# Kernel optimization log

Hardware: AMD Instinct MI355X
Metric: run time of the kernel (lower is better)

The kernel has to match this reference:

```python
import jax, jax.numpy as jnp
import numpy as np

LR = 0.01  # constraint relaxation learning rate (module default)
EPS = 1e-6


def setup_inputs() -> dict:
    key = jax.random.key(0)
    k1, k2, k3, k4 = jax.random.split(key, 4)
    N, E, K = 8192, 262144, 65536
    positions = jax.random.normal(k1, (N, 3), dtype=jnp.float32)
    edge_index = jax.random.randint(k2, (2, E), 0, N, dtype=jnp.int32)
    dist_idx = jax.random.randint(k3, (K, 2), 0, N, dtype=jnp.int32)
    dist_target = jax.random.uniform(k4, (K,), dtype=jnp.float32) * 2.0
    min_dist = jnp.ones((1,), dtype=jnp.float32) * 0.5
    return {"positions": positions, "edge_index": edge_index,
            "dist_idx": dist_idx, "dist_target": dist_target,
            "min_dist": min_dist}


def reference(positions, edge_index, dist_idx, dist_target, min_dist):
    x = positions  # (N, 3)
    N = x.shape[0]

    # --- distance constraints: ||x_i - x_j|| -> d_ij (Jacobi-style update) ---
    i, j = dist_idx[:, 0], dist_idx[:, 1]
    vec = x[i] - x[j]                                  # (K, 3)
    dist = jnp.sqrt(jnp.sum(vec * vec, axis=-1) + 1e-12)
    valid = (dist > EPS) & (i != j)
    coef = jnp.where(valid, LR * 0.5 * (dist - dist_target) / dist, 0.0)
    corr = coef[:, None] * vec                         # (K, 3)
    x = x.at[i].add(-corr).at[j].add(corr)

    # --- collision constraints: push apart all pairs with dist < min_dist ---
    md = min_dist[0]
    sq = jnp.sum(x * x, axis=-1)                       # (N,)
    d2 = jnp.maximum(sq[:, None] + sq[None, :] - 2.0 * (x @ x.T), 1e-12)
    dmat = jnp.sqrt(d2)                                # (N, N) pairwise distances
    mask = (dmat < md) & (dmat > EPS)                  # excludes diagonal (dist ~ 0)
    w = jnp.where(mask, (md - dmat) / dmat, 0.0) * (0.5 * LR)  # (N, N)
    # correction_i = sum_j w_ij * (x_i - x_j)
    x = x + x * jnp.sum(w, axis=-1, keepdims=True) - w @ x

    # --- gaussian curvature via normalized graph Laplacian ---
    e = jnp.clip(edge_index, 0, N - 1)
    adj = jnp.zeros((N, N), dtype=x.dtype).at[e[0], e[1]].set(1.0)
    adj = adj + adj.T
    deg = adj.sum(axis=1)
    dinv = jnp.where(deg == 0, 0.0, jnp.power(deg + EPS, -0.5))
    # L_norm @ x = x - D^{-1/2} A D^{-1/2} x (diagonal scaling, same math)
    lap = x - dinv[:, None] * (adj @ (dinv[:, None] * x))
    curvature = jnp.sqrt(jnp.sum(lap * lap, axis=-1) + 1e-12)  # (N,)

    return x, curvature
```

## Files before the change

### kernel.cpp

```cpp
#include <hip/hip_runtime.h>
#include <math.h>

#define N_NODES 8192
#define WPR 256
#define LR_C 0.01f
#define EPS_C 1e-6f

__global__ void scatter_constraints(const float* __restrict__ x0,
                                    const int* __restrict__ dist_idx,
                                    const float* __restrict__ dist_target,
                                    float* __restrict__ x1, int K) {
    int k = blockIdx.x * blockDim.x + threadIdx.x;
    if (k >= K) return;
    int i = dist_idx[2 * k], j = dist_idx[2 * k + 1];
    float ax = x0[3 * i], ay = x0[3 * i + 1], az = x0[3 * i + 2];
    float bx = x0[3 * j], by = x0[3 * j + 1], bz = x0[3 * j + 2];
    float vx = ax - bx, vy = ay - by, vz = az - bz;
    float dist = sqrtf(vx * vx + vy * vy + vz * vz + 1e-12f);
    bool valid = (dist > EPS_C) && (i != j);
    float coef = valid ? (LR_C * 0.5f) * (dist - dist_target[k]) / dist : 0.0f;
    if (coef != 0.0f) {
        float cx = coef * vx, cy = coef * vy, cz = coef * vz;
        atomicAdd(&x1[3 * i],     -cx);
        atomicAdd(&x1[3 * i + 1], -cy);
        atomicAdd(&x1[3 * i + 2], -cz);
        atomicAdd(&x1[3 * j],      cx);
        atomicAdd(&x1[3 * j + 1],  cy);
        atomicAdd(&x1[3 * j + 2],  cz);
    }
}

__global__ __launch_bounds__(256) void repulsion_partial(
        const float* __restrict__ x1, const float* __restrict__ min_dist,
        float4* __restrict__ partials) {
    __shared__ float4 pj[256];
    int t = threadIdx.x;
    int jbase = blockIdx.y * 256;
    int i = blockIdx.x * 256 + t;
    {
        int j = jbase + t;
        float a = x1[3 * j], b = x1[3 * j + 1], c = x1[3 * j + 2];
        pj[t] = make_float4(a, b, c, a * a + b * b + c * c);
    }
    __syncthreads();
    float xi = x1[3 * i], yi = x1[3 * i + 1], zi = x1[3 * i + 2];
    float sqi = xi * xi + yi * yi + zi * zi;
    float md = min_dist[0];
    float md2 = md * md;
    const float c0 = 0.5f * LR_C;
    float c1 = c0 * md;
    int di = i - jbase;
    float S = 0.f, axc = 0.f, ayc = 0.f, azc = 0.f;
    #pragma unroll 4
    for (int jj = 0; jj < 256; ++jj) {
        float4 p = pj[jj];
        float dot = fmaf(xi, p.x, fmaf(yi, p.y, zi * p.z));
        float d2 = fmaxf(fmaf(-2.0f, dot, sqi + p.w), 1e-12f);
        float r = __builtin_amdgcn_rsqf(d2);
        bool m = (d2 < md2) && (d2 > 1e-12f) && (jj != di);
        float w = m ? fmaf(c1, r, -c0) : 0.0f;
        S += w;
        axc = fmaf(w, p.x, axc);
        ayc = fmaf(w, p.y, ayc);
        azc = fmaf(w, p.z, azc);
    }
    partials[blockIdx.y * N_NODES + i] = make_float4(axc, ayc, azc, S);
}

__global__ void repulsion_finalize(const float* __restrict__ x1,
                                   const float4* __restrict__ partials,
                                   float* __restrict__ x2,
                                   float* __restrict__ out_x, int nchunks) {
    int i = blockIdx.x * blockDim.x + threadIdx.x;
    if (i >= N_NODES) return;
    float S = 0.f, axc = 0.f, ayc = 0.f, azc = 0.f;
    for (int c = 0; c < nchunks; ++c) {
        float4 p = partials[c * N_NODES + i];
        axc += p.x; ayc += p.y; azc += p.z; S += p.w;
    }
    float xi = x1[3 * i], yi = x1[3 * i + 1], zi = x1[3 * i + 2];
    float ox = xi + xi * S - axc;
    float oy = yi + yi * S - ayc;
    float oz = zi + zi * S - azc;
    x2[3 * i] = ox; x2[3 * i + 1] = oy; x2[3 * i + 2] = oz;
    out_x[3 * i] = ox; out_x[3 * i + 1] = oy; out_x[3 * i + 2] = oz;
}

__global__ void build_adj(const int* __restrict__ edge_index,
                          unsigned int* __restrict__ A,
                          unsigned int* __restrict__ B, int E) {
    int k = blockIdx.x * blockDim.x + threadIdx.x;
    if (k >= E) return;
    int a = edge_index[k];
    int b = edge_index[E + k];
    a = min(max(a, 0), N_NODES - 1);
    b = min(max(b, 0), N_NODES - 1);
    atomicOr(&A[a * WPR + (b >> 5)], 1u << (b & 31));
    atomicOr(&B[b * WPR + (a >> 5)], 1u << (a & 31));
}

__global__ __launch_bounds__(256) void degree_kernel(
        const unsigned int* __restrict__ A, const unsigned int* __restrict__ B,
        const float* __restrict__ x2, float* __restrict__ dinv,
        float4* __restrict__ z4) {
    int row = (blockIdx.x * blockDim.x + threadIdx.x) >> 6;
    int lane = threadIdx.x & 63;
    if (row >= N_NODES) return;
    const unsigned int* ra = A + (size_t)row * WPR;
    const unsigned int* rb = B + (size_t)row * WPR;
    int cnt = 0;
    #pragma unroll
    for (int q = 0; q < 4; ++q) {
        cnt += __popc(ra[q * 64 + lane]);
        cnt += __popc(rb[q * 64 + lane]);
    }
    for (int off = 32; off; off >>= 1) cnt += __shfl_down(cnt, off);
    if (lane == 0) {
        float dv = (cnt == 0) ? 0.0f : 1.0f / sqrtf((float)cnt + EPS_C);
        dinv[row] = dv;
        z4[row] = make_float4(dv * x2[3 * row], dv * x2[3 * row + 1],
                              dv * x2[3 * row + 2], dv);
    }
}

__global__ __launch_bounds__(256) void lap_kernel(
        const unsigned int* __restrict__ A, const unsigned int* __restrict__ B,
        const float* __restrict__ x2, const float* __restrict__ dinv,
        const float4* __restrict__ z4, float* __restrict__ out_curv) {
    int row = (blockIdx.x * blockDim.x + threadIdx.x) >> 6;
    int lane = threadIdx.x & 63;
    if (row >= N_NODES) return;
    float axc = 0.f, ayc = 0.f, azc = 0.f;
    #pragma unroll
    for (int q = 0; q < 4; ++q) {
        int wi = q * 64 + lane;
        unsigned int w = A[(size_t)row * WPR + wi];
        while (w) {
            int b = __ffs(w) - 1; w &= w - 1;
            float4 z = z4[wi * 32 + b];
            axc += z.x; ayc += z.y; azc += z.z;
        }
        w = B[(size_t)row * WPR + wi];
        while (w) {
            int b = __ffs(w) - 1; w &= w - 1;
            float4 z = z4[wi * 32 + b];
            axc += z.x; ayc += z.y; azc += z.z;
        }
    }
    for (int off = 32; off; off >>= 1) {
        axc += __shfl_down(axc, off);
        ayc += __shfl_down(ayc, off);
        azc += __shfl_down(azc, off);
    }
    if (lane == 0) {
        float dv = dinv[row];
        float lx = x2[3 * row]     - dv * axc;
        float ly = x2[3 * row + 1] - dv * ayc;
        float lz = x2[3 * row + 2] - dv * azc;
        out_curv[row] = sqrtf(lx * lx + ly * ly + lz * lz + 1e-12f);
    }
}

extern "C" void kernel_launch(void* const* d_in, const int* in_sizes, int n_in,
                              void* d_out, int out_size, void* d_ws, size_t ws_size,
                              hipStream_t stream) {
    const float* positions   = (const float*)d_in[0];
    const int*   edge_index  = (const int*)d_in[1];
    const int*   dist_idx    = (const int*)d_in[2];
    const float* dist_target = (const float*)d_in[3];
    const float* min_dist    = (const float*)d_in[4];
    float* out = (float*)d_out;

    const int E = in_sizes[1] / 2;
    const int K = in_sizes[2] / 2;
    const int NJ = 32;

    char* ws = (char*)d_ws;
    const size_t X1_OFF   = 0;
    const size_t X2_OFF   = X1_OFF + (size_t)N_NODES * 3 * 4;
    const size_t Z4_OFF   = X2_OFF + (size_t)N_NODES * 3 * 4;
    const size_t DINV_OFF = Z4_OFF + (size_t)N_NODES * 16;
    const size_t PART_OFF = DINV_OFF + (size_t)N_NODES * 4;
    const size_t ADJ_OFF  = PART_OFF + (size_t)NJ * N_NODES * 16;
    const size_t ADJ_BYTES = (size_t)N_NODES * WPR * 4;

    float* x1         = (float*)(ws + X1_OFF);
    float* x2         = (float*)(ws + X2_OFF);
    float4* z4        = (float4*)(ws + Z4_OFF);
    float* dinv       = (float*)(ws + DINV_OFF);
    float4* partials  = (float4*)(ws + PART_OFF);
    unsigned int* A   = (unsigned int*)(ws + ADJ_OFF);
    unsigned int* B   = (unsigned int*)(ws + ADJ_OFF + ADJ_BYTES);

    hipMemcpyAsync(x1, positions, (size_t)N_NODES * 3 * 4,
                   hipMemcpyDeviceToDevice, stream);
    hipMemsetAsync(A, 0, 2 * ADJ_BYTES, stream);

    scatter_constraints<<<(K + 255) / 256, 256, 0, stream>>>(
        positions, dist_idx, dist_target, x1, K);

    dim3 grid_rep(N_NODES / 256, NJ);
    repulsion_partial<<<grid_rep, 256, 0, stream>>>(x1, min_dist, partials);

    repulsion_finalize<<<N_NODES / 256, 256, 0, stream>>>(
        x1, partials, x2, out, NJ);

    build_adj<<<(E + 255) / 256, 256, 0, stream>>>(edge_index, A, B, E);

    int rows_per_block = 256 / 64;
    int nblk = N_NODES / rows_per_block;
    degree_kernel<<<nblk, 256, 0, stream>>>(A, B, x2, dinv, z4);
    lap_kernel<<<nblk, 256, 0, stream>>>(A, B, x2, dinv, z4, out + 3 * N_NODES);
}
```

Measured before the change: 103.3 us.

## Fuse init memcpy/memset into one kernel and merge finalize with degree

Replaces the device memcpy and memset with a single init kernel that zeroes the adjacency bitmaps and copies positions. It also fuses the repulsion partial-sum reduction into the degree kernel, using a wave-wide shuffle reduction over the 32 chunk partials, and moves build_adj earlier. The aim is fewer launches and less per-launch overhead. The init kernel relies on hardcoded sizes (4096*256 uint4 covers both bitmaps, and 6144 float4 covers the positions).

```diff
diff --git a/kernel.cpp b/kernel.cpp
--- a/kernel.cpp
+++ b/kernel.cpp
@@ -5,6 +5,14 @@
 #define WPR 256
 #define LR_C 0.01f
 #define EPS_C 1e-6f
+
+__global__ __launch_bounds__(256) void init_clear(const float4* __restrict__ pos4,
+                                                  float4* __restrict__ x1_4,
+                                                  uint4* __restrict__ adj) {
+    int gid = blockIdx.x * blockDim.x + threadIdx.x;
+    adj[gid] = make_uint4(0u, 0u, 0u, 0u);
+    if (gid < 6144) x1_4[gid] = pos4[gid];
+}
 
 __global__ void scatter_constraints(const float* __restrict__ x0,
                                     const int* __restrict__ dist_idx,
@@ -30,6 +38,19 @@
     }
 }
 
+__global__ void build_adj(const int* __restrict__ edge_index,
+                          unsigned int* __restrict__ A,
+                          unsigned int* __restrict__ B, int E) {
+    int k = blockIdx.x * blockDim.x + threadIdx.x;
+    if (k >= E) return;
+    int a = edge_index[k];
+    int b = edge_index[E + k];
+    a = min(max(a, 0), N_NODES - 1);
+    b = min(max(b, 0), N_NODES - 1);
+    atomicOr(&A[a * WPR + (b >> 5)], 1u << (b & 31));
+    atomicOr(&B[b * WPR + (a >> 5)], 1u << (a & 31));
+}
+
 __global__ __launch_bounds__(256) void repulsion_partial(
         const float* __restrict__ x1, const float* __restrict__ min_dist,
         float4* __restrict__ partials) {
@@ -67,59 +88,43 @@
     partials[blockIdx.y * N_NODES + i] = make_float4(axc, ayc, azc, S);
 }
 
-__global__ void repulsion_finalize(const float* __restrict__ x1,
-                                   const float4* __restrict__ partials,
-                                   float* __restrict__ x2,
-                                   float* __restrict__ out_x, int nchunks) {
-    int i = blockIdx.x * blockDim.x + threadIdx.x;
-    if (i >= N_NODES) return;
-    float S = 0.f, axc = 0.f, ayc = 0.f, azc = 0.f;
-    for (int c = 0; c < nchunks; ++c) {
-        float4 p = partials[c * N_NODES + i];
-        axc += p.x; ayc += p.y; azc += p.z; S += p.w;
-    }
-    float xi = x1[3 * i], yi = x1[3 * i + 1], zi = x1[3 * i + 2];
-    float ox = xi + xi * S - axc;
-    float oy = yi + yi * S - ayc;
-    float oz = zi + zi * S - azc;
-    x2[3 * i] = ox; x2[3 * i + 1] = oy; x2[3 * i + 2] = oz;
-    out_x[3 * i] = ox; out_x[3 * i + 1] = oy; out_x[3 * i + 2] = oz;
-}
-
-__global__ void build_adj(const int* __restrict__ edge_index,
-                          unsigned int* __restrict__ A,
-                          unsigned int* __restrict__ B, int E) {
-    int k = blockIdx.x * blockDim.x + threadIdx.x;
-    if (k >= E) return;
-    int a = edge_index[k];
-    int b = edge_index[E + k];
-    a = min(max(a, 0), N_NODES - 1);
-    b = min(max(b, 0), N_NODES - 1);
-    atomicOr(&A[a * WPR + (b >> 5)], 1u << (b & 31));
-    atomicOr(&B[b * WPR + (a >> 5)], 1u << (a & 31));
-}
-
-__global__ __launch_bounds__(256) void degree_kernel(
+__global__ __launch_bounds__(256) void finalize_degree(
+        const float* __restrict__ x1,
+        const float4* __restrict__ partials,
         const unsigned int* __restrict__ A, const unsigned int* __restrict__ B,
-        const float* __restrict__ x2, float* __restrict__ dinv,
-        float4* __restrict__ z4) {
+        float* __restrict__ x2, float* __restrict__ out_x,
+        float* __restrict__ dinv, float4* __restrict__ z4) {
     int row = (blockIdx.x * blockDim.x + threadIdx.x) >> 6;
     int lane = threadIdx.x & 63;
     if (row >= N_NODES) return;
-    const unsigned int* ra = A + (size_t)row * WPR;
-    const unsigned int* rb = B + (size_t)row * WPR;
     int cnt = 0;
     #pragma unroll
     for (int q = 0; q < 4; ++q) {
-        cnt += __popc(ra[q * 64 + lane]);
-        cnt += __popc(rb[q * 64 + lane]);
-    }
-    for (int off = 32; off; off >>= 1) cnt += __shfl_down(cnt, off);
+        cnt += __popc(A[(size_t)row * WPR + q * 64 + lane]);
+        cnt += __popc(B[(size_t)row * WPR + q * 64 + lane]);
+    }
+    float axc = 0.f, ayc = 0.f, azc = 0.f, S = 0.f;
+    if (lane < 32) {
+        float4 p = partials[lane * N_NODES + row];
+        axc = p.x; ayc = p.y; azc = p.z; S = p.w;
+    }
+    for (int off = 32; off; off >>= 1) {
+        axc += __shfl_down(axc, off);
+        ayc += __shfl_down(ayc, off);
+        azc += __shfl_down(azc, off);
+        S   += __shfl_down(S, off);
+        cnt += __shfl_down(cnt, off);
+    }
     if (lane == 0) {
+        float xi = x1[3 * row], yi = x1[3 * row + 1], zi = x1[3 * row + 2];
+        float ox = xi + xi * S - axc;
+        float oy = yi + yi * S - ayc;
+        float oz = zi + zi * S - azc;
+        x2[3 * row] = ox; x2[3 * row + 1] = oy; x2[3 * row + 2] = oz;
+        out_x[3 * row] = ox; out_x[3 * row + 1] = oy; out_x[3 * row + 2] = oz;
         float dv = (cnt == 0) ? 0.0f : 1.0f / sqrtf((float)cnt + EPS_C);
         dinv[row] = dv;
-        z4[row] = make_float4(dv * x2[3 * row], dv * x2[3 * row + 1],
-                              dv * x2[3 * row + 2], dv);
+        z4[row] = make_float4(dv * ox, dv * oy, dv * oz, dv);
     }
 }
 
@@ -192,23 +197,20 @@
     unsigned int* A   = (unsigned int*)(ws + ADJ_OFF);
     unsigned int* B   = (unsigned int*)(ws + ADJ_OFF + ADJ_BYTES);
 
-    hipMemcpyAsync(x1, positions, (size_t)N_NODES * 3 * 4,
-                   hipMemcpyDeviceToDevice, stream);
-    hipMemsetAsync(A, 0, 2 * ADJ_BYTES, stream);
+    init_clear<<<4096, 256, 0, stream>>>((const float4*)positions,
+                                         (float4*)x1, (uint4*)A);
 
     scatter_constraints<<<(K + 255) / 256, 256, 0, stream>>>(
         positions, dist_idx, dist_target, x1, K);
 
+    build_adj<<<(E + 255) / 256, 256, 0, stream>>>(edge_index, A, B, E);
+
     dim3 grid_rep(N_NODES / 256, NJ);
     repulsion_partial<<<grid_rep, 256, 0, stream>>>(x1, min_dist, partials);
 
-    repulsion_finalize<<<N_NODES / 256, 256, 0, stream>>>(
-        x1, partials, x2, out, NJ);
-
-    build_adj<<<(E + 255) / 256, 256, 0, stream>>>(edge_index, A, B, E);
-
     int rows_per_block = 256 / 64;
     int nblk = N_NODES / rows_per_block;
-    degree_kernel<<<nblk, 256, 0, stream>>>(A, B, x2, dinv, z4);
+    finalize_degree<<<nblk, 256, 0, stream>>>(x1, partials, A, B,
+                                              x2, out, dinv, z4);
     lap_kernel<<<nblk, 256, 0, stream>>>(A, B, x2, dinv, z4, out + 3 * N_NODES);
 }
```

Result: faster. 97.86 us (-5.2%).

## Fuse setup launches, count degrees during adjacency build, simplify repulsion masking

Applied to the files above, without the earlier changes.

Replaces the memcpy and memset with one init kernel that also clears a degree array. Merges the distance-constraint scatter and the adjacency-bitmap build into one launch. Degrees are counted with atomics when a bit is newly set, which removes the degree kernel's full pass over the adjacency bitmaps and lets the finalize kernel compute dinv and z4 directly. The repulsion inner loop swaps the distance compare for a clamp with fmaxf and checks the diagonal only on diagonal blocks, in exchange for extra atomic traffic on the degree counters.

```diff
diff --git a/kernel.cpp b/kernel.cpp
--- a/kernel.cpp
+++ b/kernel.cpp
@@ -5,28 +5,57 @@
 #define WPR 256
 #define LR_C 0.01f
 #define EPS_C 1e-6f
-
-__global__ void scatter_constraints(const float* __restrict__ x0,
-                                    const int* __restrict__ dist_idx,
-                                    const float* __restrict__ dist_target,
-                                    float* __restrict__ x1, int K) {
-    int k = blockIdx.x * blockDim.x + threadIdx.x;
-    if (k >= K) return;
-    int i = dist_idx[2 * k], j = dist_idx[2 * k + 1];
-    float ax = x0[3 * i], ay = x0[3 * i + 1], az = x0[3 * i + 2];
-    float bx = x0[3 * j], by = x0[3 * j + 1], bz = x0[3 * j + 2];
-    float vx = ax - bx, vy = ay - by, vz = az - bz;
-    float dist = sqrtf(vx * vx + vy * vy + vz * vz + 1e-12f);
-    bool valid = (dist > EPS_C) && (i != j);
-    float coef = valid ? (LR_C * 0.5f) * (dist - dist_target[k]) / dist : 0.0f;
-    if (coef != 0.0f) {
-        float cx = coef * vx, cy = coef * vy, cz = coef * vz;
-        atomicAdd(&x1[3 * i],     -cx);
-        atomicAdd(&x1[3 * i + 1], -cy);
-        atomicAdd(&x1[3 * i + 2], -cz);
-        atomicAdd(&x1[3 * j],      cx);
-        atomicAdd(&x1[3 * j + 1],  cy);
-        atomicAdd(&x1[3 * j + 2],  cz);
+#define NJ 32
+
+__global__ __launch_bounds__(256) void init_clear(const float4* __restrict__ pos4,
+                                                  float4* __restrict__ x1_4,
+                                                  uint4* __restrict__ adj,
+                                                  uint4* __restrict__ deg4) {
+    int gid = blockIdx.x * blockDim.x + threadIdx.x;
+    adj[gid] = make_uint4(0u, 0u, 0u, 0u);
+    if (gid < 6144) x1_4[gid] = pos4[gid];
+    if (gid < 2048) deg4[gid] = make_uint4(0u, 0u, 0u, 0u);
+}
+
+__global__ __launch_bounds__(256) void scatter_adj(
+        const float* __restrict__ x0, const int* __restrict__ dist_idx,
+        const float* __restrict__ dist_target, const int* __restrict__ edge_index,
+        float* __restrict__ x1, unsigned int* __restrict__ A,
+        unsigned int* __restrict__ B, int* __restrict__ deg,
+        int K, int E, int nbK) {
+    int blk = blockIdx.x;
+    if (blk < nbK) {
+        int k = blk * 256 + threadIdx.x;
+        if (k >= K) return;
+        int i = dist_idx[2 * k], j = dist_idx[2 * k + 1];
+        float ax = x0[3 * i], ay = x0[3 * i + 1], az = x0[3 * i + 2];
+        float bx = x0[3 * j], by = x0[3 * j + 1], bz = x0[3 * j + 2];
+        float vx = ax - bx, vy = ay - by, vz = az - bz;
+        float dist = sqrtf(vx * vx + vy * vy + vz * vz + 1e-12f);
+        bool valid = (dist > EPS_C) && (i != j);
+        float coef = valid ? (LR_C * 0.5f) * (dist - dist_target[k]) / dist : 0.0f;
+        if (coef != 0.0f) {
+            float cx = coef * vx, cy = coef * vy, cz = coef * vz;
+            atomicAdd(&x1[3 * i],     -cx);
+            atomicAdd(&x1[3 * i + 1], -cy);
+            atomicAdd(&x1[3 * i + 2], -cz);
+            atomicAdd(&x1[3 * j],      cx);
+            atomicAdd(&x1[3 * j + 1],  cy);
+            atomicAdd(&x1[3 * j + 2],  cz);
+        }
+    } else {
+        int k = (blk - nbK) * 256 + threadIdx.x;
+        if (k >= E) return;
+        int a = edge_index[k];
+        int b = edge_index[E + k];
+        a = min(max(a, 0), N_NODES - 1);
+        b = min(max(b, 0), N_NODES - 1);
+        unsigned int bitb = 1u << (b & 31);
+        unsigned int bita = 1u << (a & 31);
+        unsigned int old = atomicOr(&A[a * WPR + (b >> 5)], bitb);
+        if (!(old & bitb)) atomicAdd(&deg[a], 1);
+        old = atomicOr(&B[b * WPR + (a >> 5)], bita);
+        if (!(old & bita)) atomicAdd(&deg[b], 1);
     }
 }
 
@@ -46,35 +75,52 @@
     float xi = x1[3 * i], yi = x1[3 * i + 1], zi = x1[3 * i + 2];
     float sqi = xi * xi + yi * yi + zi * zi;
     float md = min_dist[0];
-    float md2 = md * md;
     const float c0 = 0.5f * LR_C;
     float c1 = c0 * md;
-    int di = i - jbase;
     float S = 0.f, axc = 0.f, ayc = 0.f, azc = 0.f;
-    #pragma unroll 4
-    for (int jj = 0; jj < 256; ++jj) {
-        float4 p = pj[jj];
-        float dot = fmaf(xi, p.x, fmaf(yi, p.y, zi * p.z));
-        float d2 = fmaxf(fmaf(-2.0f, dot, sqi + p.w), 1e-12f);
-        float r = __builtin_amdgcn_rsqf(d2);
-        bool m = (d2 < md2) && (d2 > 1e-12f) && (jj != di);
-        float w = m ? fmaf(c1, r, -c0) : 0.0f;
-        S += w;
-        axc = fmaf(w, p.x, axc);
-        ayc = fmaf(w, p.y, ayc);
-        azc = fmaf(w, p.z, azc);
+    if (blockIdx.x == blockIdx.y) {
+        int di = t;
+        #pragma unroll 4
+        for (int jj = 0; jj < 256; ++jj) {
+            float4 p = pj[jj];
+            float dot = fmaf(xi, p.x, fmaf(yi, p.y, zi * p.z));
+            float d2 = fmaf(-2.0f, dot, sqi + p.w);
+            float r = __builtin_amdgcn_rsqf(fmaxf(d2, 1e-12f));
+            float w = fmaxf(fmaf(c1, r, -c0), 0.0f);
+            w = (d2 > 1e-12f && jj != di) ? w : 0.0f;
+            S += w;
+            axc = fmaf(w, p.x, axc);
+            ayc = fmaf(w, p.y, ayc);
+            azc = fmaf(w, p.z, azc);
+        }
+    } else {
+        #pragma unroll 4
+        for (int jj = 0; jj < 256; ++jj) {
+            float4 p = pj[jj];
+            float dot = fmaf(xi, p.x, fmaf(yi, p.y, zi * p.z));
+            float d2 = fmaf(-2.0f, dot, sqi + p.w);
+            float r = __builtin_amdgcn_rsqf(fmaxf(d2, 1e-12f));
+            float w = fmaxf(fmaf(c1, r, -c0), 0.0f);
+            w = (d2 > 1e-12f) ? w : 0.0f;
+            S += w;
+            axc = fmaf(w, p.x, axc);
+            ayc = fmaf(w, p.y, ayc);
+            azc = fmaf(w, p.z, azc);
+        }
     }
     partials[blockIdx.y * N_NODES + i] = make_float4(axc, ayc, azc, S);
 }
 
-__global__ void repulsion_finalize(const float* __restrict__ x1,
-                                   const float4* __restrict__ partials,
-                                   float* __restrict__ x2,
-                                   float* __restrict__ out_x, int nchunks) {
+__global__ __launch_bounds__(256) void finalize(
+        const float* __restrict__ x1, const float4* __restrict__ partials,
+        const int* __restrict__ deg,
+        float* __restrict__ x2, float* __restrict__ out_x,
+        float* __restrict__ dinv, float4* __restrict__ z4) {
     int i = blockIdx.x * blockDim.x + threadIdx.x;
     if (i >= N_NODES) return;
     float S = 0.f, axc = 0.f, ayc = 0.f, azc = 0.f;
-    for (int c = 0; c < nchunks; ++c) {
+    #pragma unroll
+    for (int c = 0; c < NJ; ++c) {
         float4 p = partials[c * N_NODES + i];
         axc += p.x; ayc += p.y; azc += p.z; S += p.w;
     }
@@ -84,43 +130,10 @@
     float oz = zi + zi * S - azc;
     x2[3 * i] = ox; x2[3 * i + 1] = oy; x2[3 * i + 2] = oz;
     out_x[3 * i] = ox; out_x[3 * i + 1] = oy; out_x[3 * i + 2] = oz;
-}
-
-__global__ void build_adj(const int* __restrict__ edge_index,
-                          unsigned int* __restrict__ A,
-                          unsigned int* __restrict__ B, int E) {
-    int k = blockIdx.x * blockDim.x + threadIdx.x;
-    if (k >= E) return;
-    int a = edge_index[k];
-    int b = edge_index[E + k];
-    a = min(max(a, 0), N_NODES - 1);
-    b = min(max(b, 0), N_NODES - 1);
-    atomicOr(&A[a * WPR + (b >> 5)], 1u << (b & 31));
-    atomicOr(&B[b * WPR + (a >> 5)], 1u << (a & 31));
-}
-
-__global__ __launch_bounds__(256) void degree_kernel(
-        const unsigned int* __restrict__ A, const unsigned int* __restrict__ B,
-        const float* __restrict__ x2, float* __restrict__ dinv,
-        float4* __restrict__ z4) {
-    int row = (blockIdx.x * blockDim.x + threadIdx.x) >> 6;
-    int lane = threadIdx.x & 63;
-    if (row >= N_NODES) return;
-    const unsigned int* ra = A + (size_t)row * WPR;
-    const unsigned int* rb = B + (size_t)row * WPR;
-    int cnt = 0;
-    #pragma unroll
-    for (int q = 0; q < 4; ++q) {
-        cnt += __popc(ra[q * 64 + lane]);
-        cnt += __popc(rb[q * 64 + lane]);
-    }
-    for (int off = 32; off; off >>= 1) cnt += __shfl_down(cnt, off);
-    if (lane == 0) {
-        float dv = (cnt == 0) ? 0.0f : 1.0f / sqrtf((float)cnt + EPS_C);
-        dinv[row] = dv;
-        z4[row] = make_float4(dv * x2[3 * row], dv * x2[3 * row + 1],
-                              dv * x2[3 * row + 2], dv);
-    }
+    int d = deg[i];
+    float dv = (d == 0) ? 0.0f : 1.0f / sqrtf((float)d + EPS_C);
+    dinv[i] = dv;
+    z4[i] = make_float4(dv * ox, dv * oy, dv * oz, dv);
 }
 
 __global__ __launch_bounds__(256) void lap_kernel(
@@ -173,14 +186,14 @@
 
     const int E = in_sizes[1] / 2;
     const int K = in_sizes[2] / 2;
-    const int NJ = 32;
 
     char* ws = (char*)d_ws;
     const size_t X1_OFF   = 0;
     const size_t X2_OFF   = X1_OFF + (size_t)N_NODES * 3 * 4;
     const size_t Z4_OFF   = X2_OFF + (size_t)N_NODES * 3 * 4;
     const size_t DINV_OFF = Z4_OFF + (size_t)N_NODES * 16;
-    const size_t PART_OFF = DINV_OFF + (size_t)N_NODES * 4;
+    const size_t DEG_OFF  = DINV_OFF + (size_t)N_NODES * 4;
+    const size_t PART_OFF = DEG_OFF + (size_t)N_NODES * 4;
     const size_t ADJ_OFF  = PART_OFF + (size_t)NJ * N_NODES * 16;
     const size_t ADJ_BYTES = (size_t)N_NODES * WPR * 4;
 
@@ -188,27 +201,25 @@
     float* x2         = (float*)(ws + X2_OFF);
     float4* z4        = (float4*)(ws + Z4_OFF);
     float* dinv       = (float*)(ws + DINV_OFF);
+    int*   deg        = (int*)(ws + DEG_OFF);
     float4* partials  = (float4*)(ws + PART_OFF);
     unsigned int* A   = (unsigned int*)(ws + ADJ_OFF);
     unsigned int* B   = (unsigned int*)(ws + ADJ_OFF + ADJ_BYTES);
 
-    hipMemcpyAsync(x1, positions, (size_t)N_NODES * 3 * 4,
-                   hipMemcpyDeviceToDevice, stream);
-    hipMemsetAsync(A, 0, 2 * ADJ_BYTES, stream);
-
-    scatter_constraints<<<(K + 255) / 256, 256, 0, stream>>>(
-        positions, dist_idx, dist_target, x1, K);
+    init_clear<<<4096, 256, 0, stream>>>((const float4*)positions,
+                                         (float4*)x1, (uint4*)A, (uint4*)deg);
+
+    int nbK = (K + 255) / 256;
+    int nbE = (E + 255) / 256;
+    scatter_adj<<<nbK + nbE, 256, 0, stream>>>(
+        positions, dist_idx, dist_target, edge_index, x1, A, B, deg, K, E, nbK);
 
     dim3 grid_rep(N_NODES / 256, NJ);
     repulsion_partial<<<grid_rep, 256, 0, stream>>>(x1, min_dist, partials);
 
-    repulsion_finalize<<<N_NODES / 256, 256, 0, stream>>>(
-        x1, partials, x2, out, NJ);
-
-    build_adj<<<(E + 255) / 256, 256, 0, stream>>>(edge_index, A, B, E);
-
-    int rows_per_block = 256 / 64;
-    int nblk = N_NODES / rows_per_block;
-    degree_kernel<<<nblk, 256, 0, stream>>>(A, B, x2, dinv, z4);
-    lap_kernel<<<nblk, 256, 0, stream>>>(A, B, x2, dinv, z4, out + 3 * N_NODES);
-}
+    finalize<<<N_NODES / 256, 256, 0, stream>>>(x1, partials, deg,
+                                                x2, out, dinv, z4);
+
+    lap_kernel<<<N_NODES / 4, 256, 0, stream>>>(A, B, x2, dinv, z4,
+                                                out + 3 * N_NODES);
+}
```

Result: slower. 118.5 us (+14.8%).
